# Optimization experiments

Hardware: AMD Instinct MI355X
Metric: run time of the kernel (lower is better)

Reference implementation:

```python
import jax, jax.numpy as jnp
import numpy as np

N_NODES = 1024      # nNodes
N_EDGES = 4096      # nEdges
N_FACTORS = 64      # input feature dim (rows of kernel / paths)
BATCH = 256
NNZ_PER_ROW = 32    # nonzeros per kernel row -> iter = count_nonzero = 32 exactly
N_SOURCES = 16


def setup_inputs() -> dict:
    key = jax.random.key(0)
    k1, k2 = jax.random.split(key, 2)
    x = jax.random.normal(k1, (BATCH, N_FACTORS), dtype=jnp.float32)

    rng = np.random.default_rng(0)
    lin = rng.choice(N_NODES * N_NODES, size=N_EDGES, replace=False)
    # Edges[e] = (col, row): original scatters node_prop[i, Edges[e][1], Edges[e][0]] = paths[i][e]
    edges = np.stack([lin % N_NODES, lin // N_NODES], axis=1).astype(np.int64)

    sources = np.sort(rng.choice(N_NODES, size=N_SOURCES, replace=False)).astype(np.int64)

    # kernel ("paths") with exactly NNZ_PER_ROW nonzeros per row, so the
    # data-dependent propagation depth count_nonzero(paths[i]) == NNZ_PER_ROW
    cols = np.argsort(rng.random((N_FACTORS, N_EDGES)), axis=1)[:, :NNZ_PER_ROW]
    mask = np.zeros((N_FACTORS, N_EDGES), dtype=np.float32)
    mask[np.arange(N_FACTORS)[:, None], cols] = 1.0
    dense = np.asarray(jax.random.normal(k2, (N_FACTORS, N_EDGES), dtype=jnp.float32)) * 0.1
    kernel = jnp.asarray(dense * mask)

    return {
        "x": x,
        "kernel": kernel,
        "edges": jnp.asarray(edges),
        "sources": jnp.asarray(sources),
    }


def reference(x, kernel, edges, sources):
    F, E = kernel.shape
    N = N_NODES

    # scatter-build per-factor adjacency: node_prop[i, dst, src] = kernel[i, e]
    node_prop = jnp.zeros((F, N, N), x.dtype).at[:, edges[:, 1], edges[:, 0]].set(kernel)
    # row 0 fixed so each column sums to 1
    node_prop = node_prop.at[:, 0, :].set(1.0 - node_prop.sum(axis=1))

    source_flow = jnp.zeros((N,), x.dtype).at[sources].set(1.0)

    # data-dependent propagation depth per factor
    iters = jnp.count_nonzero(kernel, axis=1)  # [F], == NNZ_PER_ROW by construction

    # prop_flow[i] is linear in factor[i]; propagate the unit source vector per factor
    V0 = jnp.broadcast_to(source_flow, (F, N))

    def step(V, t):
        Vn = jnp.einsum('fij,fj->fi', node_prop, V)
        return jnp.where(t < iters[:, None], Vn, V), None

    V, _ = jax.lax.scan(step, V0, jnp.arange(NNZ_PER_ROW))

    # subtract factor[i] at every source node: W[i] = V[i] - 1_{sources}
    W = V - source_flow  # [F, N]

    prop_flows = x @ W        # [B, N]  (sum over factors of scaled propagated flows)
    recon = x @ kernel        # [B, E]  linear-combination reconstruction
    return prop_flows, recon
```

## Files before the change

### kernel.cpp

```cpp
#include <hip/hip_runtime.h>
#include <hip/hip_bf16.h>

#define NNODES   1024
#define NEDGES   4096
#define NFACT    64
#define NBATCH   256
#define NSRC     16
#define MAXNNZ   64
#define MAXITER  32

#define RECON_BLOCKS 512
#define FLOWS_BLOCKS 128

__global__ __launch_bounds__(256) void k1(
    const float* __restrict__ kern,
    const int*   __restrict__ edges,
    const int*   __restrict__ sources,
    const float* __restrict__ x,
    float*       __restrict__ W,
    float*       __restrict__ out)
{
    if (blockIdx.x >= NFACT) {
        int r  = blockIdx.x - NFACT;
        int e4 = (r & 3) * 256 + threadIdx.x;
        int b0 = (r >> 2) * 2;
        const float4* Kv  = (const float4*)kern;
        const float*  xr0 = x + b0 * NFACT;
        const float*  xr1 = xr0 + NFACT;
        float4 a0 = {0.f,0.f,0.f,0.f}, a1 = {0.f,0.f,0.f,0.f};
        #pragma unroll 4
        for (int k = 0; k < NFACT; ++k) {
            float4 kv = Kv[k * (NEDGES/4) + e4];
            float x0 = xr0[k], x1 = xr1[k];
            a0.x += x0*kv.x; a0.y += x0*kv.y; a0.z += x0*kv.z; a0.w += x0*kv.w;
            a1.x += x1*kv.x; a1.y += x1*kv.y; a1.z += x1*kv.z; a1.w += x1*kv.w;
        }
        float4* o4 = (float4*)(out + NBATCH * NNODES);
        o4[ b0      * (NEDGES/4) + e4] = a0;
        o4[(b0 + 1) * (NEDGES/4) + e4] = a1;
        return;
    }

    __shared__ float v_lds[NNODES];
    __shared__ float wbuf[MAXNNZ];
    __shared__ int   srcbuf[MAXNNZ];
    __shared__ int   dstbuf[MAXNNZ];
    __shared__ float c_lds[MAXNNZ];
    __shared__ int   cnt;

    const int f = blockIdx.x;
    const int t = threadIdx.x;

    if (t == 0) cnt = 0;
    __syncthreads();

    const float4* kern4 = (const float4*)(kern + f * NEDGES);
    #pragma unroll
    for (int i = 0; i < NEDGES/4/256; ++i) {
        int e4 = t + i * 256;
        float4 kv = kern4[e4];
        float vals[4] = {kv.x, kv.y, kv.z, kv.w};
        #pragma unroll
        for (int c = 0; c < 4; ++c) {
            if (vals[c] != 0.f) {
                int slot = atomicAdd(&cnt, 1);
                if (slot < MAXNNZ) {
                    wbuf[slot]   = vals[c];
                    int e        = e4 * 4 + c;
                    srcbuf[slot] = edges[2*e];
                    dstbuf[slot] = edges[2*e + 1];
                }
            }
        }
    }
    __syncthreads();

    const int nnz = min(cnt, MAXNNZ);
    const int T   = min(nnz, MAXITER);

    for (int n = t; n < NNODES; n += 256) v_lds[n] = 0.f;
    __syncthreads();

    if (t < 64) {
        const bool  active = (t < nnz);
        const float w_e = active ? wbuf[t]   : 0.f;
        const int   src = active ? srcbuf[t] : -1;
        const int   dst = active ? dstbuf[t] : -1;

        unsigned long long gmask = 0ull;
        for (int e2 = 0; e2 < nnz; ++e2)
            if (dstbuf[e2] == src) gmask |= (1ull << e2);

        float val = 0.f;
        for (int s = 0; s < NSRC; ++s)
            if (sources[s] == src) val = 1.f;
        float S = (float)NSRC;

        unsigned long long anybad =
            __ballot(active && (src == 0 || dst == 0)) |
            __ballot(__popcll(gmask) > 1);

        if (T > 0) {
            float c_fin = 0.f, v0_fin = 0.f;
            if (anybad == 0ull) {
                const int   gidx = gmask ? (__ffsll(gmask) - 1) : t;
                const float gsel = gmask ? 1.f : 0.f;
                float c = 0.f;
                for (int it = 0; it < T; ++it) {
                    c = w_e * val;
                    float g = __shfl(c, gidx);
                    val = gsel * g;
                }
                float a = c;
                #pragma unroll
                for (int o = 32; o >= 1; o >>= 1) a += __shfl_xor(a, o);
                c_fin = c; v0_fin = S - a;
            } else {
                float c = 0.f, v0 = 0.f;
                for (int it = 0; it < T; ++it) {
                    c = w_e * val;
                    c_lds[t] = c;
                    float a = c;
                    float b = (dst == 0) ? c : 0.f;
                    #pragma unroll
                    for (int o = 32; o >= 1; o >>= 1) {
                        a += __shfl_xor(a, o);
                        b += __shfl_xor(b, o);
                    }
                    v0 = S - a;
                    S  = S - b;
                    float nv = 0.f;
                    unsigned long long m = gmask;
                    while (m) { int i = __ffsll(m) - 1; nv += c_lds[i]; m &= m - 1; }
                    val = (src == 0) ? v0 : nv;
                }
                c_fin = c; v0_fin = v0;
            }
            if (t == 0) v_lds[0] = v0_fin;
            if (active && dst != 0) atomicAdd(&v_lds[dst], c_fin);
        } else {
            if (t < NSRC) v_lds[sources[t]] = 1.f;
        }
    }
    __syncthreads();
    if (t < NSRC) atomicAdd(&v_lds[sources[t]], -1.f);
    __syncthreads();

    ((float4*)(W + f * NNODES))[t] = ((const float4*)v_lds)[t];
}

__global__ __launch_bounds__(256) void k2(
    const float* __restrict__ x,
    const float* __restrict__ W,
    float*       __restrict__ out)
{
    const int b0 = blockIdx.x * 2;
    const int t  = threadIdx.x;
    const float4* Wv  = (const float4*)W;
    const float*  xr0 = x + b0 * NFACT;
    const float*  xr1 = xr0 + NFACT;
    float4 a0 = {0.f,0.f,0.f,0.f}, a1 = {0.f,0.f,0.f,0.f};
    #pragma unroll 4
    for (int k = 0; k < NFACT; ++k) {
        float4 wv = Wv[k * (NNODES/4) + t];
        float x0 = xr0[k], x1 = xr1[k];
        a0.x += x0*wv.x; a0.y += x0*wv.y; a0.z += x0*wv.z; a0.w += x0*wv.w;
        a1.x += x1*wv.x; a1.y += x1*wv.y; a1.z += x1*wv.z; a1.w += x1*wv.w;
    }
    float4* o4 = (float4*)out;
    o4[ b0      * (NNODES/4) + t] = a0;
    o4[(b0 + 1) * (NNODES/4) + t] = a1;
}

extern "C" void kernel_launch(void* const* d_in, const int* in_sizes, int n_in,
                              void* d_out, int out_size, void* d_ws, size_t ws_size,
                              hipStream_t stream) {
    const float* x       = (const float*)d_in[0];
    const float* kern    = (const float*)d_in[1];
    const int*   edges   = (const int*)d_in[2];
    const int*   sources = (const int*)d_in[3];
    float* out = (float*)d_out;
    float* W   = (float*)d_ws;

    k1<<<NFACT + RECON_BLOCKS, 256, 0, stream>>>(kern, edges, sources, x, W, out);
    k2<<<FLOWS_BLOCKS, 256, 0, stream>>>(x, W, out);
}
```

Baseline: 83.30 us.

## Compute recon as sparse dot products over nonzero kernel factors per edge

```diff
diff --git a/kernel.cpp b/kernel.cpp
--- a/kernel.cpp
+++ b/kernel.cpp
@@ -9,7 +9,8 @@
 #define MAXNNZ   64
 #define MAXITER  32
 
-#define RECON_BLOCKS 512
+#define PROP_BLOCKS  64
+#define RECON_BLOCKS 128
 #define FLOWS_BLOCKS 128
 
 __global__ __launch_bounds__(256) void k1(
@@ -20,24 +21,35 @@
     float*       __restrict__ W,
     float*       __restrict__ out)
 {
-    if (blockIdx.x >= NFACT) {
-        int r  = blockIdx.x - NFACT;
-        int e4 = (r & 3) * 256 + threadIdx.x;
-        int b0 = (r >> 2) * 2;
-        const float4* Kv  = (const float4*)kern;
-        const float*  xr0 = x + b0 * NFACT;
-        const float*  xr1 = xr0 + NFACT;
-        float4 a0 = {0.f,0.f,0.f,0.f}, a1 = {0.f,0.f,0.f,0.f};
-        #pragma unroll 4
-        for (int k = 0; k < NFACT; ++k) {
-            float4 kv = Kv[k * (NEDGES/4) + e4];
-            float x0 = xr0[k], x1 = xr1[k];
-            a0.x += x0*kv.x; a0.y += x0*kv.y; a0.z += x0*kv.z; a0.w += x0*kv.w;
-            a1.x += x1*kv.x; a1.y += x1*kv.y; a1.z += x1*kv.z; a1.w += x1*kv.w;
+    const int t = threadIdx.x;
+
+    if (blockIdx.x >= PROP_BLOCKS) {
+        const int r  = blockIdx.x - PROP_BLOCKS;
+        const int e  = r * 32 + (t & 31);
+        const int b0 = (t >> 5) * 32;
+
+        unsigned long long mask = 0ull;
+        #pragma unroll 8
+        for (int f = 0; f < NFACT; ++f) {
+            if (kern[f * NEDGES + e] != 0.0f) mask |= (1ull << f);
         }
-        float4* o4 = (float4*)(out + NBATCH * NNODES);
-        o4[ b0      * (NEDGES/4) + e4] = a0;
-        o4[(b0 + 1) * (NEDGES/4) + e4] = a1;
+
+        float* o = out + NBATCH * NNODES;
+        if (mask == 0ull) {
+            for (int i = 0; i < 32; ++i) o[(b0 + i) * NEDGES + e] = 0.0f;
+        } else {
+            for (int i = 0; i < 32; ++i) {
+                const int b = b0 + i;
+                float acc = 0.0f;
+                unsigned long long m = mask;
+                while (m) {
+                    int f = __ffsll(m) - 1;
+                    m &= m - 1;
+                    acc += kern[f * NEDGES + e] * x[b * NFACT + f];
+                }
+                o[b * NEDGES + e] = acc;
+            }
+        }
         return;
     }
 
@@ -49,7 +61,6 @@
     __shared__ int   cnt;
 
     const int f = blockIdx.x;
-    const int t = threadIdx.x;
 
     if (t == 0) cnt = 0;
     __syncthreads();
@@ -182,6 +193,6 @@
     float* out = (float*)d_out;
     float* W   = (float*)d_ws;
 
-    k1<<<NFACT + RECON_BLOCKS, 256, 0, stream>>>(kern, edges, sources, x, W, out);
+    k1<<<PROP_BLOCKS + RECON_BLOCKS, 256, 0, stream>>>(kern, edges, sources, x, W, out);
     k2<<<FLOWS_BLOCKS, 256, 0, stream>>>(x, W, out);
 }
```

Result: slower. 86.97 us (+4.4%).
